# Performance work log

Hardware: AMD Instinct MI355X
Metric: run time of the kernel (lower is better)

## Reference

```python
import jax, jax.numpy as jnp
import numpy as np

N_NODES = 512
HEADS = 4
CO = 64        # per-head out channels (PyG GATConv out_channels)
NEG_SLOPE = 0.2  # PyG GATConv default negative_slope


def setup_inputs() -> dict:
    key = jax.random.key(0)
    k0, k1, k2, k3, k4 = jax.random.split(key, 5)
    B, C, T, N = 8, 64, 12, N_NODES
    E = 8192
    x = jax.random.normal(k0, (B, C, T, N), dtype=jnp.float32)
    edge_index = jax.random.randint(k1, (2, E), 0, N, dtype=jnp.int32)
    # learned params of GATConv(in=64, out=64, heads=4, concat=False)
    W = jax.random.normal(k2, (C, HEADS * CO), dtype=jnp.float32) / np.sqrt(C).astype(np.float32)
    att_src = jax.random.normal(k3, (HEADS, CO), dtype=jnp.float32) * 0.1
    att_dst = jax.random.normal(k4, (HEADS, CO), dtype=jnp.float32) * 0.1
    bias = jnp.zeros((CO,), dtype=jnp.float32)
    return {"x": x, "edge_index": edge_index, "W": W,
            "att_src": att_src, "att_dst": att_dst, "bias": bias}


def reference(x, edge_index, W, att_src, att_dst, bias):
    # x: [B, C, T, N] -> batch of G = B*T graphs, all sharing edge_index.
    B, C, T, N = x.shape
    H, Co = att_src.shape
    G = B * T
    xg = x.transpose(0, 2, 3, 1).reshape(G, N, C)              # [G,N,C]
    h = (xg @ W).reshape(G, N, H, Co)                          # [G,N,H,Co]
    a_src = jnp.einsum('gnhc,hc->gnh', h, att_src)             # [G,N,H]
    a_dst = jnp.einsum('gnhc,hc->gnh', h, att_dst)             # [G,N,H]
    # add self loops (PyG GATConv default)
    loops = jnp.arange(N, dtype=edge_index.dtype)
    src = jnp.concatenate([edge_index[0], loops])              # [E']
    dst = jnp.concatenate([edge_index[1], loops])              # [E']
    # attention logits per edge, leading edge axis for segment ops
    logits = jax.nn.leaky_relu(a_src[:, src] + a_dst[:, dst], NEG_SLOPE)  # [G,E',H]
    logits = logits.transpose(1, 0, 2)                         # [E',G,H]
    m = jax.ops.segment_max(logits, dst, num_segments=N)       # [N,G,H]
    e = jnp.exp(logits - m[dst])
    s = jax.ops.segment_sum(e, dst, num_segments=N)            # [N,G,H]
    alpha = e / s[dst]                                         # [E',G,H]  (dropout off: eval)
    msg = alpha[..., None] * h[:, src].transpose(1, 0, 2, 3)   # [E',G,H,Co]
    out = jax.ops.segment_sum(msg, dst, num_segments=N)        # [N,G,H,Co]
    out = out.mean(axis=2) + bias                              # [N,G,Co]  concat=False -> head mean
    out = out.transpose(1, 0, 2).reshape(B, T, N, Co)          # [B,T,N,Co]
    return out.transpose(0, 3, 1, 2)                           # [B,Co,T,N]
```

## Files before the change

### kernel.cpp

```cpp
#include <hip/hip_runtime.h>

#define B_  8
#define C_  64
#define T_  12
#define N_  512
#define E_  8192
#define H_  4
#define CO_ 64
#define G_  (B_ * T_)
#define EP_ (E_ + N_)
#define MAXDEG 128
#define MDW    48
#define POISON 0xAAAAAAAAu

typedef __bf16 bf16x8 __attribute__((ext_vector_type(8)));
typedef unsigned short usx8 __attribute__((ext_vector_type(8)));
typedef float  f32x4  __attribute__((ext_vector_type(4)));

static __device__ __forceinline__ unsigned short f2bf(float f) {
    unsigned int u = __float_as_uint(f);
    return (unsigned short)((u + 0x7fffu + ((u >> 16) & 1u)) >> 16);
}
static __device__ __forceinline__ float lo16f(unsigned int u) {
    return (float)__builtin_bit_cast(_Float16, (unsigned short)(u & 0xffffu));
}
static __device__ __forceinline__ float hi16f(unsigned int u) {
    return (float)__builtin_bit_cast(_Float16, (unsigned short)(u >> 16));
}

__global__ __launch_bounds__(256) void k_prep(
    const float* __restrict__ x, const int* __restrict__ ei,
    const float* __restrict__ W,
    const float* __restrict__ att_src, const float* __restrict__ att_dst,
    unsigned short* __restrict__ xtb, float* __restrict__ as_, float* __restrict__ ad_,
    unsigned int* __restrict__ cnt, int* __restrict__ srclist,
    unsigned short* __restrict__ Wfrag)
{
    int bid = blockIdx.x, tid = threadIdx.x;

    if (bid >= 1536) {
        if (bid < 1568) {
            int e = (bid - 1536) * 256 + tid;
            int d = ei[E_ + e], s = ei[e];
            unsigned int pos = atomicAdd(&cnt[d], 1u) - POISON;
            srclist[d * MAXDEG + pos] = s;
        } else {
            int base = (bid - 1568) * 2048;
            #pragma unroll
            for (int it = 0; it < 8; ++it) {
                int idx = base + it * 256 + tid;
                int c  = idx >> 8, r = idx & 255;
                int hh = r >> 6,  co = r & 63;
                int k  = hh * 64 + c;
                int ks = k >> 5, kq = (k >> 3) & 3, j = k & 7;
                int nt = co >> 4, l = kq * 16 + (co & 15);
                Wfrag[(size_t)((ks * 4 + nt) * 64 + l) * 8 + j] = f2bf(W[idx]);
            }
        }
        return;
    }

    __shared__ float xs[64][33];
    __shared__ float Wls[64][4], Wld[64][4];
    __shared__ float sa[32][9];

    int lane = tid & 63, q = tid >> 6;

    {
        const float4* W4 = reinterpret_cast<const float4*>(W);
        const float4* A4 = reinterpret_cast<const float4*>(att_src);
        const float4* D4 = reinterpret_cast<const float4*>(att_dst);
        float4 uu = A4[lane];
        float4 vv = D4[lane];
        #pragma unroll
        for (int it = 0; it < 16; ++it) {
            int idx4 = tid + it * 256;
            float4 w = W4[idx4];
            float s1 = w.x*uu.x + w.y*uu.y + w.z*uu.z + w.w*uu.w;
            float s2 = w.x*vv.x + w.y*vv.y + w.z*vv.z + w.w*vv.w;
            #pragma unroll
            for (int off = 1; off < 16; off <<= 1) {
                s1 += __shfl_xor(s1, off, 64);
                s2 += __shfl_xor(s2, off, 64);
            }
            if ((lane & 15) == 0) {
                Wls[q + it * 4][lane >> 4] = s1;
                Wld[q + it * 4][lane >> 4] = s2;
            }
        }
    }

    int g  = bid >> 4, tl = bid & 15;
    int b  = g / T_, t = g - b * T_;
    int n0 = tl * 32;

    int n = tid & 31, cq = tid >> 5;

    #pragma unroll
    for (int i = 0; i < 8; ++i) {
        int c = cq * 8 + i;
        xs[c][n] = x[((size_t)(b * C_ + c) * T_ + t) * N_ + n0 + n];
    }
    __syncthreads();

    {
        const float (*Wp)[4] = (cq >> 2) ? Wld : Wls;
        int h = cq & 3;
        float s = 0.f;
        for (int c = 0; c < 64; ++c) s += xs[c][n] * Wp[c][h];
        sa[n][cq] = s;
    }

    #pragma unroll
    for (int i = 0; i < 8; ++i) {
        int n2 = q * 8 + i;
        xtb[((size_t)(g * N_ + n0 + n2)) * 64 + lane] = f2bf(xs[lane][n2]);
    }
    __syncthreads();

    int n3 = tid >> 3, k = tid & 7;
    float v = sa[n3][k];
    float* dst = (k >> 2) ? ad_ : as_;
    dst[((size_t)(g * N_ + n0 + n3)) * 4 + (k & 3)] = v;
}

__global__ __launch_bounds__(256, 6) void k_fused(
    const unsigned short* __restrict__ xtb, const float* __restrict__ as_,
    const float* __restrict__ ad_,
    const unsigned int* __restrict__ cnt, const int* __restrict__ srclist,
    const unsigned short* __restrict__ Wfrag, const float* __restrict__ bias,
    float* __restrict__ out)
{
    __shared__ __align__(16) char lds[12032];
    unsigned int*   wbu = reinterpret_cast<unsigned int*>(lds + 8192);
    unsigned short* ssu = reinterpret_cast<unsigned short*>(lds + 11264);
    float (*tl)[65] = reinterpret_cast<float (*)[65]>(lds);

    int bid  = blockIdx.x;
    int xcd  = bid & 7, rest = bid >> 3;
    int gq   = rest % 12, tile = rest / 12;
    int g    = xcd * 12 + gq;
    int n0   = tile * 16;
    int b    = g / T_, t = g - b * T_;
    int tid  = threadIdx.x;
    int wave = tid >> 6, lane = tid & 63;
    int fslot = tid >> 5;
    int t32  = tid & 31;
    int hp   = t32 & 1;
    int fp   = t32 >> 1;
    int hl   = lane & 31;
    int ch2  = hl * 2;

    const unsigned short* xg = xtb + ((size_t)g * N_) * 64 + ch2;
    const float2* as2 = reinterpret_cast<const float2*>(as_) + (size_t)g * N_ * 2;
    const float2* ad2 = reinterpret_cast<const float2*>(ad_) + (size_t)g * N_ * 2;

    struct Stage {
        int dt, dtfr, scnt, node;
        int se[3];
        float2 sav[3];
        float2 adv;
    };

    auto do_stage = [&](int qq, Stage& S) {
        int node = n0 + fslot * 2 + qq;
        int dg = (int)(cnt[node] - POISON);
        dg = min(dg, MDW - 2);
        S.dt = dg + 1;
        int pm = max(S.dt, __shfl_xor(S.dt, 32, 64));
        pm = __builtin_amdgcn_readfirstlane(pm);
        S.dtfr = (pm + 7) & ~7;
        S.node = node;
        S.adv  = ad2[(size_t)node * 2 + hp];
        S.scnt = 0;
        #pragma unroll
        for (int i = 0; i < 3; ++i) {
            int e = fp + i * 16;
            if (e < S.dt) {
                int s = (e < dg) ? srclist[node * MAXDEG + e] : node;
                S.se[i]  = s;
                S.sav[i] = as2[(size_t)s * 2 + hp];
                S.scnt = i + 1;
            }
        }
    };

    auto do_fill = [&](const Stage& S) {
        #pragma unroll
        for (int i = 0; i < 3; ++i) {
            if (i < S.scnt) {
                int e = fp + i * 16;
                float v0 = S.sav[i].x + S.adv.x; v0 = v0 > 0.f ? v0 : 0.2f * v0;
                float v1 = S.sav[i].y + S.adv.y; v1 = v1 > 0.f ? v1 : 0.2f * v1;
                auto ph = __builtin_amdgcn_cvt_pkrtz(__expf(v0), __expf(v1));
                wbu[(fslot * MDW + e) * 2 + hp] = __builtin_bit_cast(unsigned int, ph);
                if (hp == 0) ssu[fslot * MDW + e] = (unsigned short)S.se[i];
            }
        }
        for (int e = S.dt + t32; e < S.dtfr; e += 32) {
            wbu[(fslot * MDW + e) * 2 + 0] = 0u;
            wbu[(fslot * MDW + e) * 2 + 1] = 0u;
            ssu[fslot * MDW + e] = (unsigned short)S.node;
        }
    };

    Stage cur, nxt;
    do_stage(0, cur);
    do_fill(cur);

    for (int p = 0; p < 2; ++p) {
        if (p < 1) do_stage(1, nxt);

        const unsigned short* srow = ssu + fslot * MDW;
        const uint2* wrow = reinterpret_cast<const uint2*>(wbu + fslot * MDW * 2);
        int dtfr = cur.dtfr;

        float zA0=0.f, zA1=0.f, zA2=0.f, zA3=0.f;
        float zB0=0.f, zB1=0.f, zB2=0.f, zB3=0.f;
        float s0=0.f, s1=0.f, s2=0.f, s3=0.f;

        uint4 ssv = *reinterpret_cast<const uint4*>(srow);
        unsigned int xv[8];
        {
            unsigned int sw4[4] = {ssv.x, ssv.y, ssv.z, ssv.w};
            #pragma unroll
            for (int j = 0; j < 8; ++j) {
                unsigned int si = (j & 1) ? (sw4[j >> 1] >> 16) : (sw4[j >> 1] & 0xffffu);
                xv[j] = *reinterpret_cast<const unsigned int*>(xg + (size_t)si * 64);
            }
        }
        for (int e = 8; e <= dtfr; e += 8) {
            unsigned int xv2[8];
            if (e < dtfr) {
                uint4 ssv2 = *reinterpret_cast<const uint4*>(srow + e);
                unsigned int sw4[4] = {ssv2.x, ssv2.y, ssv2.z, ssv2.w};
                #pragma unroll
                for (int j = 0; j < 8; ++j) {
                    unsigned int si = (j & 1) ? (sw4[j >> 1] >> 16) : (sw4[j >> 1] & 0xffffu);
                    xv2[j] = *reinterpret_cast<const unsigned int*>(xg + (size_t)si * 64);
                }
            }
            const uint2* wp = wrow + (e - 8);
            #pragma unroll
            for (int j = 0; j < 8; ++j) {
                uint2 wq = wp[j];
                float wa = lo16f(wq.x), wb_ = hi16f(wq.x);
                float wc = lo16f(wq.y), wd  = hi16f(wq.y);
                float x0 = __uint_as_float(xv[j] << 16);
                float x1 = __uint_as_float(xv[j] & 0xffff0000u);
                zA0 += wa * x0;  zB0 += wa * x1;  s0 += wa;
                zA1 += wb_ * x0; zB1 += wb_ * x1; s1 += wb_;
                zA2 += wc * x0;  zB2 += wc * x1;  s2 += wc;
                zA3 += wd * x0;  zB3 += wd * x1;  s3 += wd;
            }
            if (e < dtfr) {
                #pragma unroll
                for (int j = 0; j < 8; ++j) xv[j] = xv2[j];
            }
        }

        int nl = cur.node - n0;

        if (p < 1) { do_fill(nxt); }

        float r0 = __builtin_amdgcn_rcpf(s0), r1 = __builtin_amdgcn_rcpf(s1);
        float r2 = __builtin_amdgcn_rcpf(s2), r3 = __builtin_amdgcn_rcpf(s3);
        unsigned int sw = (unsigned int)((nl & 7) << 4);
        unsigned int o0 = (unsigned int)(nl * 512 + ch2 * 2);
        unsigned int p0 = (unsigned int)f2bf(zA0 * r0) | ((unsigned int)f2bf(zB0 * r0) << 16);
        unsigned int p1 = (unsigned int)f2bf(zA1 * r1) | ((unsigned int)f2bf(zB1 * r1) << 16);
        unsigned int p2 = (unsigned int)f2bf(zA2 * r2) | ((unsigned int)f2bf(zB2 * r2) << 16);
        unsigned int p3 = (unsigned int)f2bf(zA3 * r3) | ((unsigned int)f2bf(zB3 * r3) << 16);
        *reinterpret_cast<unsigned int*>(lds + ((o0 +   0) ^ sw)) = p0;
        *reinterpret_cast<unsigned int*>(lds + ((o0 + 128) ^ sw)) = p1;
        *reinterpret_cast<unsigned int*>(lds + ((o0 + 256) ^ sw)) = p2;
        *reinterpret_cast<unsigned int*>(lds + ((o0 + 384) ^ sw)) = p3;

        if (p < 1) cur = nxt;
    }

    __syncthreads();

    int m = lane & 15, quad = lane >> 4;
    unsigned int swr = (unsigned int)((m & 7) << 4);
    int nt = wave;

    f32x4 acc = (f32x4){0.f, 0.f, 0.f, 0.f};
    #pragma unroll
    for (int ks = 0; ks < 8; ++ks) {
        unsigned int ro = (unsigned int)(m * 512 + quad * 16 + ks * 64);
        uint4 za = *reinterpret_cast<const uint4*>(lds + (ro ^ swr));
        bf16x8 a = __builtin_bit_cast(bf16x8, za);
        usx8 ub = *reinterpret_cast<const usx8*>(
            Wfrag + (size_t)(((ks * 4 + nt) * 64 + lane) * 8));
        bf16x8 bw = __builtin_bit_cast(bf16x8, ub);
        acc = __builtin_amdgcn_mfma_f32_16x16x32_bf16(a, bw, acc, 0, 0, 0);
    }
    __syncthreads();

    {
        int co = nt * 16 + m;
        float bv = bias[co];
        #pragma unroll
        for (int rr = 0; rr < 4; ++rr) {
            int row = quad * 4 + rr;
            tl[row][co] = 0.25f * acc[rr] + bv;
        }
    }
    __syncthreads();

    {
        int nl2 = tid & 15, cb = tid >> 4;
        #pragma unroll
        for (int it = 0; it < 4; ++it) {
            int c = cb + it * 16;
            out[((size_t)(b * CO_ + c) * T_ + t) * N_ + n0 + nl2] = tl[nl2][c];
        }
    }
}

extern "C" void kernel_launch(void* const* d_in, const int* in_sizes, int n_in,
                              void* d_out, int out_size, void* d_ws, size_t ws_size,
                              hipStream_t stream) {
    const float* x       = (const float*)d_in[0];
    const int*   ei      = (const int*)  d_in[1];
    const float* W       = (const float*)d_in[2];
    const float* att_src = (const float*)d_in[3];
    const float* att_dst = (const float*)d_in[4];
    const float* bias    = (const float*)d_in[5];
    float* out = (float*)d_out;

    char* p = (char*)d_ws;
    unsigned short* xtb = (unsigned short*)p; p += (size_t)G_ * N_ * C_ * sizeof(unsigned short);
    float* as_     = (float*)p;  p += (size_t)G_ * N_ * H_ * sizeof(float);
    float* ad_     = (float*)p;  p += (size_t)G_ * N_ * H_ * sizeof(float);
    unsigned short* Wfrag = (unsigned short*)p; p += 64 * 256 * sizeof(unsigned short);
    unsigned int* cnt = (unsigned int*)p; p += 512 * sizeof(unsigned int);
    int* srclist   = (int*)p;    p += N_ * MAXDEG * sizeof(int);

    k_prep  <<<1576, 256, 0, stream>>>(x, ei, W, att_src, att_dst,
                                       xtb, as_, ad_, cnt, srclist, Wfrag);
    k_fused <<<3072, 256, 0, stream>>>(xtb, as_, ad_, cnt, srclist, Wfrag, bias, out);
}
```

Baseline: 132.9 us.

## Double fused-kernel node tile to 32 and restructure attention weight precompute

The fused aggregation kernel now handles 32 destination nodes per block instead of 16. It runs four pipelined stage/fill passes and two MFMA accumulators that share each loaded W fragment, so the grid is halved and the per-block W fragment load is amortised. In the prep kernel, the W·att projection now uses a per-thread dot product over 64 elements instead of a shuffle reduction, and the x loads are issued before it so their latency overlaps. LDS use grows to about 20 KB per block, and fewer blocks mean less parallelism to hide gather latency.

```diff
diff --git a/kernel.cpp b/kernel.cpp
--- a/kernel.cpp
+++ b/kernel.cpp
@@ -66,41 +66,36 @@
 
     int lane = tid & 63, q = tid >> 6;
 
-    {
-        const float4* W4 = reinterpret_cast<const float4*>(W);
-        const float4* A4 = reinterpret_cast<const float4*>(att_src);
-        const float4* D4 = reinterpret_cast<const float4*>(att_dst);
-        float4 uu = A4[lane];
-        float4 vv = D4[lane];
-        #pragma unroll
-        for (int it = 0; it < 16; ++it) {
-            int idx4 = tid + it * 256;
-            float4 w = W4[idx4];
-            float s1 = w.x*uu.x + w.y*uu.y + w.z*uu.z + w.w*uu.w;
-            float s2 = w.x*vv.x + w.y*vv.y + w.z*vv.z + w.w*vv.w;
-            #pragma unroll
-            for (int off = 1; off < 16; off <<= 1) {
-                s1 += __shfl_xor(s1, off, 64);
-                s2 += __shfl_xor(s2, off, 64);
-            }
-            if ((lane & 15) == 0) {
-                Wls[q + it * 4][lane >> 4] = s1;
-                Wld[q + it * 4][lane >> 4] = s2;
-            }
-        }
-    }
-
     int g  = bid >> 4, tl = bid & 15;
     int b  = g / T_, t = g - b * T_;
     int n0 = tl * 32;
 
     int n = tid & 31, cq = tid >> 5;
 
+    float xv[8];
     #pragma unroll
     for (int i = 0; i < 8; ++i) {
         int c = cq * 8 + i;
-        xs[c][n] = x[((size_t)(b * C_ + c) * T_ + t) * N_ + n0 + n];
-    }
+        xv[i] = x[((size_t)(b * C_ + c) * T_ + t) * N_ + n0 + n];
+    }
+
+    {
+        float s1 = 0.f, s2 = 0.f;
+        const float4* w4 = reinterpret_cast<const float4*>(W + lane * 256 + q * 64);
+        const float4* a1 = reinterpret_cast<const float4*>(att_src + q * 64);
+        const float4* a2 = reinterpret_cast<const float4*>(att_dst + q * 64);
+        #pragma unroll
+        for (int j = 0; j < 16; ++j) {
+            float4 w = w4[j], u = a1[j], v = a2[j];
+            s1 += w.x*u.x + w.y*u.y + w.z*u.z + w.w*u.w;
+            s2 += w.x*v.x + w.y*v.y + w.z*v.z + w.w*v.w;
+        }
+        Wls[lane][q] = s1;
+        Wld[lane][q] = s2;
+    }
+
+    #pragma unroll
+    for (int i = 0; i < 8; ++i) xs[cq * 8 + i][n] = xv[i];
     __syncthreads();
 
     {
@@ -131,16 +126,16 @@
     const unsigned short* __restrict__ Wfrag, const float* __restrict__ bias,
     float* __restrict__ out)
 {
-    __shared__ __align__(16) char lds[12032];
-    unsigned int*   wbu = reinterpret_cast<unsigned int*>(lds + 8192);
-    unsigned short* ssu = reinterpret_cast<unsigned short*>(lds + 11264);
+    __shared__ __align__(16) char lds[20224];
+    unsigned int*   wbu = reinterpret_cast<unsigned int*>(lds + 16384);
+    unsigned short* ssu = reinterpret_cast<unsigned short*>(lds + 19456);
     float (*tl)[65] = reinterpret_cast<float (*)[65]>(lds);
 
     int bid  = blockIdx.x;
     int xcd  = bid & 7, rest = bid >> 3;
     int gq   = rest % 12, tile = rest / 12;
     int g    = xcd * 12 + gq;
-    int n0   = tile * 16;
+    int n0   = tile * 32;
     int b    = g / T_, t = g - b * T_;
     int tid  = threadIdx.x;
     int wave = tid >> 6, lane = tid & 63;
@@ -163,7 +158,7 @@
     };
 
     auto do_stage = [&](int qq, Stage& S) {
-        int node = n0 + fslot * 2 + qq;
+        int node = n0 + qq * 8 + fslot;
         int dg = (int)(cnt[node] - POISON);
         dg = min(dg, MDW - 2);
         S.dt = dg + 1;
@@ -208,8 +203,8 @@
     do_stage(0, cur);
     do_fill(cur);
 
-    for (int p = 0; p < 2; ++p) {
-        if (p < 1) do_stage(1, nxt);
+    for (int p = 0; p < 4; ++p) {
+        if (p < 3) do_stage(p + 1, nxt);
 
         const unsigned short* srow = ssu + fslot * MDW;
         const uint2* wrow = reinterpret_cast<const uint2*>(wbu + fslot * MDW * 2);
@@ -261,7 +256,7 @@
 
         int nl = cur.node - n0;
 
-        if (p < 1) { do_fill(nxt); }
+        if (p < 3) { do_fill(nxt); }
 
         float r0 = __builtin_amdgcn_rcpf(s0), r1 = __builtin_amdgcn_rcpf(s1);
         float r2 = __builtin_amdgcn_rcpf(s2), r3 = __builtin_amdgcn_rcpf(s3);
@@ -276,7 +271,7 @@
         *reinterpret_cast<unsigned int*>(lds + ((o0 + 256) ^ sw)) = p2;
         *reinterpret_cast<unsigned int*>(lds + ((o0 + 384) ^ sw)) = p3;
 
-        if (p < 1) cur = nxt;
+        if (p < 3) cur = nxt;
     }
 
     __syncthreads();
@@ -285,16 +280,21 @@
     unsigned int swr = (unsigned int)((m & 7) << 4);
     int nt = wave;
 
-    f32x4 acc = (f32x4){0.f, 0.f, 0.f, 0.f};
+    f32x4 acc0 = (f32x4){0.f, 0.f, 0.f, 0.f};
+    f32x4 acc1 = (f32x4){0.f, 0.f, 0.f, 0.f};
     #pragma unroll
     for (int ks = 0; ks < 8; ++ks) {
-        unsigned int ro = (unsigned int)(m * 512 + quad * 16 + ks * 64);
-        uint4 za = *reinterpret_cast<const uint4*>(lds + (ro ^ swr));
-        bf16x8 a = __builtin_bit_cast(bf16x8, za);
         usx8 ub = *reinterpret_cast<const usx8*>(
             Wfrag + (size_t)(((ks * 4 + nt) * 64 + lane) * 8));
         bf16x8 bw = __builtin_bit_cast(bf16x8, ub);
-        acc = __builtin_amdgcn_mfma_f32_16x16x32_bf16(a, bw, acc, 0, 0, 0);
+        unsigned int ro0 = (unsigned int)(m * 512 + quad * 16 + ks * 64);
+        uint4 za0 = *reinterpret_cast<const uint4*>(lds + (ro0 ^ swr));
+        acc0 = __builtin_amdgcn_mfma_f32_16x16x32_bf16(
+                   __builtin_bit_cast(bf16x8, za0), bw, acc0, 0, 0, 0);
+        unsigned int ro1 = ro0 + 16 * 512;
+        uint4 za1 = *reinterpret_cast<const uint4*>(lds + (ro1 ^ swr));
+        acc1 = __builtin_amdgcn_mfma_f32_16x16x32_bf16(
+                   __builtin_bit_cast(bf16x8, za1), bw, acc1, 0, 0, 0);
     }
     __syncthreads();
 
@@ -304,16 +304,17 @@
         #pragma unroll
         for (int rr = 0; rr < 4; ++rr) {
             int row = quad * 4 + rr;
-            tl[row][co] = 0.25f * acc[rr] + bv;
+            tl[row][co]      = 0.25f * acc0[rr] + bv;
+            tl[row + 16][co] = 0.25f * acc1[rr] + bv;
         }
     }
     __syncthreads();
 
     {
-        int nl2 = tid & 15, cb = tid >> 4;
-        #pragma unroll
-        for (int it = 0; it < 4; ++it) {
-            int c = cb + it * 16;
+        int nl2 = tid & 31, cb = tid >> 5;
+        #pragma unroll
+        for (int it = 0; it < 8; ++it) {
+            int c = cb + it * 8;
             out[((size_t)(b * CO_ + c) * T_ + t) * N_ + n0 + nl2] = tl[nl2][c];
         }
     }
@@ -340,5 +341,5 @@
 
     k_prep  <<<1576, 256, 0, stream>>>(x, ei, W, att_src, att_dst,
                                        xtb, as_, ad_, cnt, srclist, Wfrag);
-    k_fused <<<3072, 256, 0, stream>>>(xtb, as_, ad_, cnt, srclist, Wfrag, bias, out);
-}
+    k_fused <<<1536, 256, 0, stream>>>(xtb, as_, ad_, cnt, srclist, Wfrag, bias, out);
+}
```

After: 183.1 us. +37.7%, slower.
